# Performance work log

Measured on AMD Instinct MI355X. Metric: run time of the kernel, lower is better.

Reference implementation:

```python
import jax, jax.numpy as jnp
import numpy as np

N, E, C = 50000, 800000, 128
D = C // 4
EPS = 1e-5


def _bn(x, g, b):
    # training-mode BatchNorm1d over the batch (row) dimension
    mu = jnp.mean(x, axis=0)
    var = jnp.var(x, axis=0)
    return (x - mu) * jax.lax.rsqrt(var + EPS) * g + b


def _lin_bn_elu(x, w, b, g, bb):
    return jax.nn.elu(_bn(x @ w + b, g, bb))


def setup_inputs() -> dict:
    key = jax.random.key(0)
    ks = iter(jax.random.split(key, 40))
    inp = {}
    inp['node_feats'] = jax.random.normal(next(ks), (N, C), jnp.float32)
    inp['edge_feats'] = jax.random.normal(next(ks), (E, C), jnp.float32)
    inp['src'] = jax.random.randint(next(ks), (E,), 0, N)
    inp['dst'] = jax.random.randint(next(ks), (E,), 0, N)

    def add_lin(name, fi, fo):
        inp[name + '_w'] = jax.random.normal(next(ks), (fi, fo), jnp.float32) / np.sqrt(fi)
        inp[name + '_b'] = jnp.zeros((fo,), jnp.float32)

    def add_bn(name, f):
        inp[name + '_g'] = jnp.ones((f,), jnp.float32)
        inp[name + '_b'] = jnp.zeros((f,), jnp.float32)

    add_lin('pdn', C, D); add_bn('bn1n', D)
    add_lin('pde', C, D); add_bn('bn1e', D)
    add_lin('e1', 3 * D, D); add_bn('bne1', D)
    add_lin('e2', 2 * D, D); add_bn('bne2', D)
    add_lin('nm', 2 * D, D); add_bn('bnnm', D)
    add_lin('pun', D, C); add_bn('bn2n', C)
    add_lin('pue', D, C); add_bn('bn2e', C)
    return inp


def reference(node_feats, edge_feats, src, dst,
              pdn_w, pdn_b, bn1n_g, bn1n_b,
              pde_w, pde_b, bn1e_g, bn1e_b,
              e1_w, e1_b, bne1_g, bne1_b,
              e2_w, e2_b, bne2_g, bne2_b,
              nm_w, nm_b, bnnm_g, bnnm_b,
              pun_w, pun_b, bn2n_g, bn2n_b,
              pue_w, pue_b, bn2e_g, bn2e_b):
    # project down
    h_node = _lin_bn_elu(node_feats, pdn_w, pdn_b, bn1n_g, bn1n_b)  # [N,D]
    h_edge = _lin_bn_elu(edge_feats, pde_w, pde_b, bn1e_g, bn1e_b)  # [E,D]
    # ENConv: gather src/dst node features per edge
    hs = h_node[src]  # [E,D]
    hd = h_node[dst]  # [E,D]
    ex = _lin_bn_elu(jnp.concatenate([hs, hd, h_edge], axis=1), e1_w, e1_b, bne1_g, bne1_b)  # [E,D]
    m = _lin_bn_elu(jnp.concatenate([hs, ex], axis=1), e2_w, e2_b, bne2_g, bne2_b)  # [E,D]
    # scatter-mean messages to destination nodes (DGL fn.mean; isolated nodes -> 0)
    msum = jax.ops.segment_sum(m, dst, num_segments=N)
    deg = jax.ops.segment_sum(jnp.ones((E,), m.dtype), dst, num_segments=N)
    h_mean = msum / jnp.maximum(deg, 1.0)[:, None]
    ho = _lin_bn_elu(jnp.concatenate([h_node, h_mean], axis=1), nm_w, nm_b, bnnm_g, bnnm_b)  # [N,D]
    # project up + residual (dropout is identity in eval)
    node_out = jax.nn.elu(_bn(ho @ pun_w + pun_b, bn2n_g, bn2n_b) + node_feats)
    edge_out = jax.nn.elu(_bn(ex @ pue_w + pue_b, bn2e_g, bn2e_b) + edge_feats)
    return node_out, edge_out
```

## Files before the change

kernel.cpp:

```cpp
#include <hip/hip_runtime.h>
#include <hip/hip_bf16.h>

typedef unsigned int u32;
typedef unsigned short u16;

#define NN 50000
#define EE 800000
#define EPSBN 1e-5f

static constexpr size_t ALGN = 256;
static constexpr size_t align_up(size_t x){ return (x + ALGN - 1) & ~(ALGN - 1); }

static constexpr size_t OFF_ST   = 0;
static constexpr size_t OFF_MSUM = align_up(OFF_ST + 832*4);
static constexpr size_t OFF_DEG  = align_up(OFF_MSUM + (size_t)NN*32*4);
static constexpr size_t ZERO_END = align_up(OFF_DEG + (size_t)NN*4);
static constexpr size_t OFF_WF   = ZERO_END;
static constexpr size_t OFF_BF   = align_up(OFF_WF + 23552*4);
static constexpr size_t OFF_AFF  = align_up(OFF_BF + 416*4);
static constexpr size_t OFF_GB   = align_up(OFF_AFF + 832*4);
static constexpr size_t OFF_FLAG = align_up(OFF_GB + 832*4);
static constexpr size_t OFF_X1N  = align_up(OFF_FLAG + 256);
static constexpr size_t OFF_HOP  = align_up(OFF_X1N + (size_t)NN*32*4);
static constexpr size_t OFF_X1E  = align_up(OFF_HOP + (size_t)NN*32*4);
static constexpr size_t OFF_EXP  = align_up(OFF_X1E + (size_t)EE*32*2);

#define ST_1N 0
#define ST_1E 64
#define ST_E1 128
#define ST_E2 192
#define ST_NM 256
#define ST_2N 320
#define ST_2E 576
#define WF_PDN 0
#define WF_PDE 4096
#define WF_E1  8192
#define WF_E2  11264
#define WF_NM  13312
#define WF_PUN 15360
#define WF_PUE 19456
#define BF_PDN 0
#define BF_PDE 32
#define BF_E1  64
#define BF_E2  96
#define BF_NM  128
#define BF_PUN 160
#define BF_PUE 288
#define AF_1N 0
#define AF_1E 64
#define AF_E1 128
#define AF_E2 192
#define AF_NM 256
#define AF_2N 320
#define AF_2E 576

__device__ __forceinline__ float bf2f(u16 h){ return __uint_as_float(((u32)h)<<16); }
__device__ __forceinline__ u16 f2bf(float f){
  u32 u = __float_as_uint(f);
  u32 r = (u + 0x7fffu + ((u>>16)&1u)) >> 16;
  return (u16)r;
}
__device__ __forceinline__ float eluf(float x){ return x > 0.f ? x : __expf(x) - 1.f; }
__device__ __forceinline__ float wsum64(float v){
  #pragma unroll
  for (int off = 32; off; off >>= 1) v += __shfl_xor(v, off, 64);
  return v;
}

__device__ __forceinline__ void stats_flush(const float* sum, const float* ssq,
                                            float* gsum, float* gssq){
  const int lane = threadIdx.x & 63;
  float a = 0.f;
  #pragma unroll
  for (int q = 0; q < 32; q++){
    float s = wsum64(sum[q]);
    float t = wsum64(ssq[q]);
    if (lane == q)      a = s;
    if (lane == 32 + q) a = t;
  }
  if (lane < 32) atomicAdd(gsum + lane, a);
  else           atomicAdd(gssq + (lane - 32), a);
}

__device__ __forceinline__ void part_f32_affelu(const float* __restrict__ x,
    const float* __restrict__ aff, const float* __restrict__ W, float* acc){
  for (int k0 = 0; k0 < 32; k0 += 4){
    float4 v = *(const float4*)(x + k0);
    const float xv[4] = {v.x, v.y, v.z, v.w};
    #pragma unroll
    for (int i = 0; i < 4; i++){
      float h = eluf(fmaf(xv[i], aff[k0+i], aff[32+k0+i]));
      const float* wr = W + (k0+i)*32;
      #pragma unroll
      for (int j = 0; j < 32; j++) acc[j] = fmaf(h, wr[j], acc[j]);
    }
  }
}
__device__ __forceinline__ void part_mean(const float* __restrict__ x, float scale,
    const float* __restrict__ W, float* acc){
  for (int k0 = 0; k0 < 32; k0 += 4){
    float4 v = *(const float4*)(x + k0);
    const float xv[4] = {v.x, v.y, v.z, v.w};
    #pragma unroll
    for (int i = 0; i < 4; i++){
      float h = xv[i] * scale;
      const float* wr = W + (k0+i)*32;
      #pragma unroll
      for (int j = 0; j < 32; j++) acc[j] = fmaf(h, wr[j], acc[j]);
    }
  }
}
__device__ __forceinline__ void part_bf16_affelu(const u32* __restrict__ xw,
    const float* __restrict__ aff, const float* __restrict__ W, float* acc){
  for (int k0 = 0; k0 < 32; k0 += 8){
    uint4 u = *(const uint4*)(xw + k0/2);
    const u32 ww[4] = {u.x, u.y, u.z, u.w};
    #pragma unroll
    for (int i = 0; i < 4; i++){
      int k = k0 + 2*i;
      float h0 = eluf(fmaf(__uint_as_float(ww[i]<<16),          aff[k],   aff[32+k]));
      float h1 = eluf(fmaf(__uint_as_float(ww[i]&0xffff0000u),  aff[k+1], aff[32+k+1]));
      const float* wr = W + k*32;
      #pragma unroll
      for (int j = 0; j < 32; j++) acc[j] = fmaf(h0, wr[j],    acc[j]);
      #pragma unroll
      for (int j = 0; j < 32; j++) acc[j] = fmaf(h1, wr[32+j], acc[j]);
    }
  }
}
template<int BF16IN>
__device__ __forceinline__ void part_up(const void* __restrict__ xin, size_t r,
    const float* __restrict__ aff, const float* __restrict__ W, int c, float* acc){
  if (BF16IN){
    const u32* xw = ((const u32*)xin) + r*16;
    for (int k0 = 0; k0 < 32; k0 += 8){
      uint4 u = *(const uint4*)(xw + k0/2);
      const u32 ww[4] = {u.x, u.y, u.z, u.w};
      #pragma unroll
      for (int i = 0; i < 4; i++){
        int k = k0 + 2*i;
        float h0 = eluf(fmaf(__uint_as_float(ww[i]<<16),         aff[k],   aff[32+k]));
        float h1 = eluf(fmaf(__uint_as_float(ww[i]&0xffff0000u), aff[k+1], aff[32+k+1]));
        const float* wr = W + k*128 + c*32;
        #pragma unroll
        for (int j = 0; j < 32; j++) acc[j] = fmaf(h0, wr[j],     acc[j]);
        #pragma unroll
        for (int j = 0; j < 32; j++) acc[j] = fmaf(h1, wr[128+j], acc[j]);
      }
    }
  } else {
    const float* xf = ((const float*)xin) + r*32;
    for (int k0 = 0; k0 < 32; k0 += 4){
      float4 v = *(const float4*)(xf + k0);
      const float xv[4] = {v.x, v.y, v.z, v.w};
      #pragma unroll
      for (int i = 0; i < 4; i++){
        float h = eluf(fmaf(xv[i], aff[k0+i], aff[32+k0+i]));
        const float* wr = W + (k0+i)*128 + c*32;
        #pragma unroll
        for (int j = 0; j < 32; j++) acc[j] = fmaf(h, wr[j], acc[j]);
      }
    }
  }
}


__global__ void ksniff(const u16* __restrict__ p, int* __restrict__ flag){
  __shared__ int cnt;
  if (threadIdx.x == 0) cnt = 0;
  __syncthreads();
  u16 u = p[threadIdx.x];
  int e = (u >> 7) & 0xFF;
  if (e >= 97 && e <= 134) atomicAdd(&cnt, 1);
  __syncthreads();
  if (threadIdx.x == 0) *flag = (cnt >= 200) ? 1 : 0;
}

struct PrepArgs { const void* s[28]; float* d[28]; int n[28]; };
__global__ void __launch_bounds__(256) kprep(PrepArgs a, const int* __restrict__ flagp){
  const int isbf = *flagp;
  const int gid = blockIdx.x*256 + threadIdx.x;
  const int stride = gridDim.x*256;
  for (int t = 0; t < 28; t++){
    float* d = a.d[t]; int n = a.n[t];
    if (isbf){
      const u16* s = (const u16*)a.s[t];
      for (int i = gid; i < n; i += stride) d[i] = bf2f(s[i]);
    } else {
      const float* s = (const float*)a.s[t];
      for (int i = gid; i < n; i += stride) d[i] = s[i];
    }
  }
}

template<int STOREBF>
__global__ void __launch_bounds__(256) kproj(const void* __restrict__ xin,
    const float* __restrict__ W, const float* __restrict__ bias,
    void* __restrict__ xout, float* gsum, float* gssq, int nrows,
    const int* __restrict__ flagp){
  const int isbf = *flagp;
  const int gid = blockIdx.x*256 + threadIdx.x;
  const int stride = gridDim.x*256;
  float sum[32], ssq[32];
  #pragma unroll
  for (int j = 0; j < 32; j++){ sum[j] = 0.f; ssq[j] = 0.f; }
  for (int r = gid; r < nrows; r += stride){
    float acc[32];
    #pragma unroll
    for (int j = 0; j < 32; j++) acc[j] = bias[j];
    if (isbf){
      const uint4* row = (const uint4*)((const u32*)xin + (size_t)r*64);
      for (int kk = 0; kk < 16; kk++){
        uint4 u = row[kk];
        const u32 ww[4] = {u.x, u.y, u.z, u.w};
        #pragma unroll
        for (int i = 0; i < 4; i++){
          float x0 = __uint_as_float(ww[i]<<16);
          float x1 = __uint_as_float(ww[i]&0xffff0000u);
          const float* w0 = W + (kk*8 + 2*i)*32;
          #pragma unroll
          for (int j = 0; j < 32; j++) acc[j] = fmaf(x0, w0[j],    acc[j]);
          #pragma unroll
          for (int j = 0; j < 32; j++) acc[j] = fmaf(x1, w0[32+j], acc[j]);
        }
      }
    } else {
      const float* rowf = (const float*)xin + (size_t)r*128;
      for (int kk = 0; kk < 32; kk++){
        float4 v = *(const float4*)(rowf + kk*4);
        const float xv[4] = {v.x, v.y, v.z, v.w};
        #pragma unroll
        for (int i = 0; i < 4; i++){
          const float* w0 = W + (kk*4 + i)*32;
          #pragma unroll
          for (int j = 0; j < 32; j++) acc[j] = fmaf(xv[i], w0[j], acc[j]);
        }
      }
    }
    if (STOREBF){
      u32 pk[16];
      #pragma unroll
      for (int q = 0; q < 16; q++) pk[q] = (u32)f2bf(acc[2*q]) | ((u32)f2bf(acc[2*q+1])<<16);
      uint4* op = (uint4*)((u32*)xout + (size_t)r*16);
      #pragma unroll
      for (int q = 0; q < 4; q++) op[q] = make_uint4(pk[q*4], pk[q*4+1], pk[q*4+2], pk[q*4+3]);
    } else {
      float4* op = (float4*)((float*)xout + (size_t)r*32);
      #pragma unroll
      for (int q = 0; q < 8; q++)
        op[q] = make_float4(acc[q*4], acc[q*4+1], acc[q*4+2], acc[q*4+3]);
    }
    #pragma unroll
    for (int j = 0; j < 32; j++){ sum[j] += acc[j]; ssq[j] = fmaf(acc[j], acc[j], ssq[j]); }
  }
  stats_flush(sum, ssq, gsum, gssq);
}

__global__ void __launch_bounds__(256) kex(const int* __restrict__ src,
    const int* __restrict__ dst, const float* __restrict__ x1n,
    const u32* __restrict__ x1e, const float* __restrict__ a1n,
    const float* __restrict__ a1e, const float* __restrict__ W,
    const float* __restrict__ bias, u32* __restrict__ expre,
    float* gsum, float* gssq, int nrows){
  const int gid = blockIdx.x*256 + threadIdx.x;
  const int stride = gridDim.x*256;
  float sum[32], ssq[32];
  #pragma unroll
  for (int j = 0; j < 32; j++){ sum[j] = 0.f; ssq[j] = 0.f; }
  for (int r = gid; r < nrows; r += stride){
    float acc[32];
    #pragma unroll
    for (int j = 0; j < 32; j++) acc[j] = bias[j];
    int s = src[r], d = dst[r];
    part_f32_affelu(x1n + (size_t)s*32, a1n, W,        acc);
    part_f32_affelu(x1n + (size_t)d*32, a1n, W + 1024, acc);
    part_bf16_affelu(x1e + (size_t)r*16, a1e, W + 2048, acc);
    u32 pk[16];
    #pragma unroll
    for (int q = 0; q < 16; q++) pk[q] = (u32)f2bf(acc[2*q]) | ((u32)f2bf(acc[2*q+1])<<16);
    uint4* op = (uint4*)(expre + (size_t)r*16);
    #pragma unroll
    for (int q = 0; q < 4; q++) op[q] = make_uint4(pk[q*4], pk[q*4+1], pk[q*4+2], pk[q*4+3]);
    #pragma unroll
    for (int j = 0; j < 32; j++){ sum[j] += acc[j]; ssq[j] = fmaf(acc[j], acc[j], ssq[j]); }
  }
  stats_flush(sum, ssq, gsum, gssq);
}

__global__ void __launch_bounds__(256) km(const int* __restrict__ src,
    const float* __restrict__ x1n, const float* __restrict__ a1n,
    const u32* __restrict__ expre, const float* __restrict__ ae1,
    const float* __restrict__ W, const float* __restrict__ bias,
    u32* __restrict__ mpre, float* gsum, float* gssq, int nrows){
  const int gid = blockIdx.x*256 + threadIdx.x;
  const int stride = gridDim.x*256;
  float sum[32], ssq[32];
  #pragma unroll
  for (int j = 0; j < 32; j++){ sum[j] = 0.f; ssq[j] = 0.f; }
  for (int r = gid; r < nrows; r += stride){
    float acc[32];
    #pragma unroll
    for (int j = 0; j < 32; j++) acc[j] = bias[j];
    int s = src[r];
    part_f32_affelu(x1n + (size_t)s*32, a1n, W, acc);
    part_bf16_affelu(expre + (size_t)r*16, ae1, W + 1024, acc);
    u32 pk[16];
    #pragma unroll
    for (int q = 0; q < 16; q++) pk[q] = (u32)f2bf(acc[2*q]) | ((u32)f2bf(acc[2*q+1])<<16);
    uint4* op = (uint4*)(mpre + (size_t)r*16);
    #pragma unroll
    for (int q = 0; q < 4; q++) op[q] = make_uint4(pk[q*4], pk[q*4+1], pk[q*4+2], pk[q*4+3]);
    #pragma unroll
    for (int j = 0; j < 32; j++){ sum[j] += acc[j]; ssq[j] = fmaf(acc[j], acc[j], ssq[j]); }
  }
  stats_flush(sum, ssq, gsum, gssq);
}

__global__ void __launch_bounds__(256) ksc(const int* __restrict__ dst,
    const u32* __restrict__ mpre, const float* __restrict__ ae2,
    float* __restrict__ msum, float* __restrict__ deg){
  const int gid = blockIdx.x*256 + threadIdx.x;
  const int stride = gridDim.x*256;
  const u16* mp = (const u16*)mpre;
  for (int idx = gid; idx < EE*32; idx += stride){
    int e = idx >> 5, j = idx & 31;
    float v = eluf(fmaf(bf2f(mp[idx]), ae2[j], ae2[32+j]));
    int dn = dst[e];
    atomicAdd(msum + (size_t)dn*32 + j, v);
    if (j == 0) atomicAdd(deg + dn, 1.f);
  }
}

__global__ void __launch_bounds__(256) kho(const float* __restrict__ x1n,
    const float* __restrict__ a1n, const float* __restrict__ msum,
    const float* __restrict__ deg, const float* __restrict__ W,
    const float* __restrict__ bias, float* __restrict__ hopre,
    float* gsum, float* gssq, int nrows){
  const int gid = blockIdx.x*256 + threadIdx.x;
  const int stride = gridDim.x*256;
  float sum[32], ssq[32];
  #pragma unroll
  for (int j = 0; j < 32; j++){ sum[j] = 0.f; ssq[j] = 0.f; }
  for (int r = gid; r < nrows; r += stride){
    float acc[32];
    #pragma unroll
    for (int j = 0; j < 32; j++) acc[j] = bias[j];
    part_f32_affelu(x1n + (size_t)r*32, a1n, W, acc);
    float id = 1.f / fmaxf(deg[r], 1.f);
    part_mean(msum + (size_t)r*32, id, W + 1024, acc);
    float4* op = (float4*)(hopre + (size_t)r*32);
    #pragma unroll
    for (int q = 0; q < 8; q++)
      op[q] = make_float4(acc[q*4], acc[q*4+1], acc[q*4+2], acc[q*4+3]);
    #pragma unroll
    for (int j = 0; j < 32; j++){ sum[j] += acc[j]; ssq[j] = fmaf(acc[j], acc[j], ssq[j]); }
  }
  stats_flush(sum, ssq, gsum, gssq);
}

template<int BF16IN>
__global__ void __launch_bounds__(256) kup1(const void* __restrict__ xin,
    const float* __restrict__ aff, const float* __restrict__ W,
    const float* __restrict__ bias, float* __restrict__ st, int nrows){
  const int gid = blockIdx.x*256 + threadIdx.x;
  const int stride = gridDim.x*256;
  for (int c = 0; c < 4; c++){
    float sum[32], ssq[32];
    #pragma unroll
    for (int j = 0; j < 32; j++){ sum[j] = 0.f; ssq[j] = 0.f; }
    for (int r = gid; r < nrows; r += stride){
      float acc[32];
      #pragma unroll
      for (int j = 0; j < 32; j++) acc[j] = bias[c*32+j];
      part_up<BF16IN>(xin, (size_t)r, aff, W, c, acc);
      #pragma unroll
      for (int j = 0; j < 32; j++){ sum[j] += acc[j]; ssq[j] = fmaf(acc[j], acc[j], ssq[j]); }
    }
    stats_flush(sum, ssq, st + c*32, st + 128 + c*32);
  }
}

template<int BF16IN>
__global__ void __launch_bounds__(256) kup2(const void* __restrict__ xin,
    const float* __restrict__ aff_in, const float* __restrict__ W,
    const float* __restrict__ bias, const float* __restrict__ aff_out,
    const void* __restrict__ resid, void* __restrict__ out,
    size_t row_off, int nrows, const int* __restrict__ flagp){
  const int isbf = *flagp;
  const int gid = blockIdx.x*256 + threadIdx.x;
  const int stride = gridDim.x*256;
  for (int r = gid; r < nrows; r += stride){
    for (int c = 0; c < 4; c++){
      float acc[32];
      #pragma unroll
      for (int j = 0; j < 32; j++) acc[j] = bias[c*32+j];
      part_up<BF16IN>(xin, (size_t)r, aff_in, W, c, acc);
      const float* sc = aff_out + c*32;
      const float* sh = aff_out + 128 + c*32;
      if (isbf){
        const u32* rrow = (const u32*)resid + (size_t)r*64 + c*16;
        u32* orow = (u32*)out + (row_off + (size_t)r)*64 + c*16;
        u32 rw[16];
        const uint4* rp = (const uint4*)rrow;
        #pragma unroll
        for (int q = 0; q < 4; q++){
          uint4 u = rp[q];
          rw[q*4] = u.x; rw[q*4+1] = u.y; rw[q*4+2] = u.z; rw[q*4+3] = u.w;
        }
        u32 pk[16];
        #pragma unroll
        for (int q = 0; q < 16; q++){
          float o0 = eluf(fmaf(acc[2*q],   sc[2*q],   sh[2*q])   + __uint_as_float(rw[q]<<16));
          float o1 = eluf(fmaf(acc[2*q+1], sc[2*q+1], sh[2*q+1]) + __uint_as_float(rw[q]&0xffff0000u));
          pk[q] = (u32)f2bf(o0) | ((u32)f2bf(o1)<<16);
        }
        uint4* op = (uint4*)orow;
        #pragma unroll
        for (int q = 0; q < 4; q++) op[q] = make_uint4(pk[q*4], pk[q*4+1], pk[q*4+2], pk[q*4+3]);
      } else {
        const float* rrow = (const float*)resid + (size_t)r*128 + c*32;
        float* orow = (float*)out + (row_off + (size_t)r)*128 + c*32;
        #pragma unroll
        for (int q = 0; q < 8; q++){
          float4 rv = *(const float4*)(rrow + q*4);
          float o0 = eluf(fmaf(acc[q*4],   sc[q*4],   sh[q*4])   + rv.x);
          float o1 = eluf(fmaf(acc[q*4+1], sc[q*4+1], sh[q*4+1]) + rv.y);
          float o2 = eluf(fmaf(acc[q*4+2], sc[q*4+2], sh[q*4+2]) + rv.z);
          float o3 = eluf(fmaf(acc[q*4+3], sc[q*4+3], sh[q*4+3]) + rv.w);
          *(float4*)(orow + q*4) = make_float4(o0, o1, o2, o3);
        }
      }
    }
  }
}

__global__ void kfin(const float* __restrict__ st, const float* __restrict__ g,
                     const float* __restrict__ b, float* __restrict__ aff,
                     int ncols, float invcnt){
  int j = threadIdx.x;
  if (j < ncols){
    float mu  = st[j] * invcnt;
    float var = fmaxf(fmaf(-mu, mu, st[ncols+j] * invcnt), 0.f);
    float scv = g[j] * rsqrtf(var + EPSBN);
    aff[j] = scv;
    aff[ncols+j] = fmaf(-mu, scv, b[j]);
  }
}

extern "C" void kernel_launch(void* const* d_in, const int* in_sizes, int n_in,
                              void* d_out, int out_size, void* d_ws, size_t ws_size,
                              hipStream_t stream){
  (void)in_sizes; (void)n_in; (void)out_size; (void)ws_size;
  char* ws = (char*)d_ws;
  float* ST  = (float*)(ws + OFF_ST);
  float* MS  = (float*)(ws + OFF_MSUM);
  float* DG  = (float*)(ws + OFF_DEG);
  float* WF  = (float*)(ws + OFF_WF);
  float* BFp = (float*)(ws + OFF_BF);
  float* AF  = (float*)(ws + OFF_AFF);
  float* GB  = (float*)(ws + OFF_GB);
  int*   FL  = (int*)(ws + OFF_FLAG);
  float* X1N = (float*)(ws + OFF_X1N);
  float* HOP = (float*)(ws + OFF_HOP);
  u32*   X1E = (u32*)(ws + OFF_X1E);
  u32*   EXP = (u32*)(ws + OFF_EXP);

  const int* src = (const int*)d_in[2];
  const int* dst = (const int*)d_in[3];

  hipMemsetAsync(ws + OFF_ST, 0, ZERO_END - OFF_ST, stream);
  ksniff<<<1,256,0,stream>>>((const u16*)d_in[0], FL);

  PrepArgs pa;
  const int widx[7] = {4,8,12,16,20,24,28};
  const int woff[7] = {WF_PDN,WF_PDE,WF_E1,WF_E2,WF_NM,WF_PUN,WF_PUE};
  const int wlen[7] = {4096,4096,3072,2048,2048,4096,4096};
  const int bidx[7] = {5,9,13,17,21,25,29};
  const int boff[7] = {BF_PDN,BF_PDE,BF_E1,BF_E2,BF_NM,BF_PUN,BF_PUE};
  const int blen[7] = {32,32,32,32,32,128,128};
  const int gbidx[14] = {6,7,10,11,14,15,18,19,22,23,26,27,30,31};
  const int gboff[14] = {0,32,64,96,128,160,192,224,256,288,320,448,576,704};
  const int gblen[14] = {32,32,32,32,32,32,32,32,32,32,128,128,128,128};
  for (int t = 0; t < 7; t++){
    pa.s[t]   = d_in[widx[t]]; pa.d[t]   = WF  + woff[t]; pa.n[t]   = wlen[t];
    pa.s[7+t] = d_in[bidx[t]]; pa.d[7+t] = BFp + boff[t]; pa.n[7+t] = blen[t];
  }
  for (int t = 0; t < 14; t++){
    pa.s[14+t] = d_in[gbidx[t]]; pa.d[14+t] = GB + gboff[t]; pa.n[14+t] = gblen[t];
  }
  kprep<<<32,256,0,stream>>>(pa, FL);

  kproj<0><<<196,256,0,stream>>>(d_in[0], WF+WF_PDN, BFp+BF_PDN, X1N, ST+ST_1N, ST+ST_1N+32, NN, FL);
  kproj<1><<<1024,256,0,stream>>>(d_in[1], WF+WF_PDE, BFp+BF_PDE, X1E, ST+ST_1E, ST+ST_1E+32, EE, FL);
  kfin<<<1,128,0,stream>>>(ST+ST_1N, GB+0,  GB+32, AF+AF_1N, 32, 1.0f/NN);
  kfin<<<1,128,0,stream>>>(ST+ST_1E, GB+64, GB+96, AF+AF_1E, 32, 1.0f/EE);

  kex<<<1024,256,0,stream>>>(src, dst, X1N, X1E, AF+AF_1N, AF+AF_1E,
                             WF+WF_E1, BFp+BF_E1, EXP, ST+ST_E1, ST+ST_E1+32, EE);
  kfin<<<1,128,0,stream>>>(ST+ST_E1, GB+128, GB+160, AF+AF_E1, 32, 1.0f/EE);

  km<<<1024,256,0,stream>>>(src, X1N, AF+AF_1N, EXP, AF+AF_E1,
                            WF+WF_E2, BFp+BF_E2, X1E , ST+ST_E2, ST+ST_E2+32, EE);
  kfin<<<1,128,0,stream>>>(ST+ST_E2, GB+192, GB+224, AF+AF_E2, 32, 1.0f/EE);

  ksc<<<2048,256,0,stream>>>(dst, X1E, AF+AF_E2, MS, DG);

  kho<<<196,256,0,stream>>>(X1N, AF+AF_1N, MS, DG, WF+WF_NM, BFp+BF_NM, HOP,
                            ST+ST_NM, ST+ST_NM+32, NN);
  kfin<<<1,128,0,stream>>>(ST+ST_NM, GB+256, GB+288, AF+AF_NM, 32, 1.0f/NN);

  kup1<0><<<196,256,0,stream>>>(HOP, AF+AF_NM, WF+WF_PUN, BFp+BF_PUN, ST+ST_2N, NN);
  kfin<<<1,128,0,stream>>>(ST+ST_2N, GB+320, GB+448, AF+AF_2N, 128, 1.0f/NN);
  kup2<0><<<196,256,0,stream>>>(HOP, AF+AF_NM, WF+WF_PUN, BFp+BF_PUN, AF+AF_2N,
                                d_in[0], d_out, 0, NN, FL);

  kup1<1><<<1024,256,0,stream>>>(EXP, AF+AF_E1, WF+WF_PUE, BFp+BF_PUE, ST+ST_2E, EE);
  kfin<<<1,128,0,stream>>>(ST+ST_2E, GB+576, GB+704, AF+AF_2E, 128, 1.0f/EE);
  kup2<1><<<2048,256,0,stream>>>(EXP, AF+AF_E1, WF+WF_PUE, BFp+BF_PUE, AF+AF_2E,
                                 d_in[1], d_out, NN, EE, FL);
}
```

Before: 2.222 ms.

## Compute up-projection BatchNorm stats via Gram matrix instead of full matmul pass

The separate stats pass over the 32→128 up-projection is replaced by a kernel that accumulates the column sums and the 32x32 Gram matrix of the activated inputs. A small finalize kernel then derives per-output mean and variance through W^T S W. This removes a full 128-wide matmul pass over 800k edges and 50k nodes. The output kernel now computes the activated input once per row and uses nontemporal stores, and several grid sizes are raised. The Gram-based variance can lose precision through cancellation in fp32.

```diff
diff --git a/kernel.cpp b/kernel.cpp
--- a/kernel.cpp
+++ b/kernel.cpp
@@ -3,6 +3,8 @@
 
 typedef unsigned int u32;
 typedef unsigned short u16;
+typedef unsigned int u32x4 __attribute__((ext_vector_type(4)));
+typedef float f32x4 __attribute__((ext_vector_type(4)));
 
 #define NN 50000
 #define EE 800000
@@ -30,8 +32,6 @@
 #define ST_E1 128
 #define ST_E2 192
 #define ST_NM 256
-#define ST_2N 320
-#define ST_2E 576
 #define WF_PDN 0
 #define WF_PDE 4096
 #define WF_E1  8192
@@ -128,41 +128,6 @@
     }
   }
 }
-template<int BF16IN>
-__device__ __forceinline__ void part_up(const void* __restrict__ xin, size_t r,
-    const float* __restrict__ aff, const float* __restrict__ W, int c, float* acc){
-  if (BF16IN){
-    const u32* xw = ((const u32*)xin) + r*16;
-    for (int k0 = 0; k0 < 32; k0 += 8){
-      uint4 u = *(const uint4*)(xw + k0/2);
-      const u32 ww[4] = {u.x, u.y, u.z, u.w};
-      #pragma unroll
-      for (int i = 0; i < 4; i++){
-        int k = k0 + 2*i;
-        float h0 = eluf(fmaf(__uint_as_float(ww[i]<<16),         aff[k],   aff[32+k]));
-        float h1 = eluf(fmaf(__uint_as_float(ww[i]&0xffff0000u), aff[k+1], aff[32+k+1]));
-        const float* wr = W + k*128 + c*32;
-        #pragma unroll
-        for (int j = 0; j < 32; j++) acc[j] = fmaf(h0, wr[j],     acc[j]);
-        #pragma unroll
-        for (int j = 0; j < 32; j++) acc[j] = fmaf(h1, wr[128+j], acc[j]);
-      }
-    }
-  } else {
-    const float* xf = ((const float*)xin) + r*32;
-    for (int k0 = 0; k0 < 32; k0 += 4){
-      float4 v = *(const float4*)(xf + k0);
-      const float xv[4] = {v.x, v.y, v.z, v.w};
-      #pragma unroll
-      for (int i = 0; i < 4; i++){
-        float h = eluf(fmaf(xv[i], aff[k0+i], aff[32+k0+i]));
-        const float* wr = W + (k0+i)*128 + c*32;
-        #pragma unroll
-        for (int j = 0; j < 32; j++) acc[j] = fmaf(h, wr[j], acc[j]);
-      }
-    }
-  }
-}
 
 
 __global__ void ksniff(const u16* __restrict__ p, int* __restrict__ flag){
@@ -359,25 +324,103 @@
 }
 
 template<int BF16IN>
-__global__ void __launch_bounds__(256) kup1(const void* __restrict__ xin,
-    const float* __restrict__ aff, const float* __restrict__ W,
-    const float* __restrict__ bias, float* __restrict__ st, int nrows){
-  const int gid = blockIdx.x*256 + threadIdx.x;
-  const int stride = gridDim.x*256;
-  for (int c = 0; c < 4; c++){
-    float sum[32], ssq[32];
-    #pragma unroll
-    for (int j = 0; j < 32; j++){ sum[j] = 0.f; ssq[j] = 0.f; }
-    for (int r = gid; r < nrows; r += stride){
-      float acc[32];
-      #pragma unroll
-      for (int j = 0; j < 32; j++) acc[j] = bias[c*32+j];
-      part_up<BF16IN>(xin, (size_t)r, aff, W, c, acc);
-      #pragma unroll
-      for (int j = 0; j < 32; j++){ sum[j] += acc[j]; ssq[j] = fmaf(acc[j], acc[j], ssq[j]); }
-    }
-    stats_flush(sum, ssq, st + c*32, st + 128 + c*32);
-  }
+__global__ void __launch_bounds__(256) ksyrk(const void* __restrict__ xin,
+    const float* __restrict__ aff, float* __restrict__ s1g,
+    float* __restrict__ s2g, int nrows){
+  __shared__ float hL[256*34];
+  const int t = threadIdx.x;
+  const int i0 = (t >> 4) << 1;
+  const int j0 = (t & 15) << 1;
+  float s1[32];
+  #pragma unroll
+  for (int k = 0; k < 32; k++) s1[k] = 0.f;
+  float c00 = 0.f, c01 = 0.f, c10 = 0.f, c11 = 0.f;
+  const int stride = gridDim.x*256;
+  for (int base = blockIdx.x*256; base < nrows; base += stride){
+    int r = base + t;
+    int nv = nrows - base; if (nv > 256) nv = 256;
+    __syncthreads();
+    if (r < nrows){
+      float* hrow = hL + t*34;
+      if (BF16IN){
+        const uint4* xp = (const uint4*)((const u32*)xin + (size_t)r*16);
+        #pragma unroll
+        for (int q2 = 0; q2 < 4; q2++){
+          uint4 u = xp[q2];
+          const u32 ww[4] = {u.x, u.y, u.z, u.w};
+          #pragma unroll
+          for (int i = 0; i < 4; i++){
+            int k = q2*8 + 2*i;
+            float h0 = eluf(fmaf(__uint_as_float(ww[i]<<16),         aff[k],   aff[32+k]));
+            float h1 = eluf(fmaf(__uint_as_float(ww[i]&0xffff0000u), aff[k+1], aff[32+k+1]));
+            hrow[k] = h0; hrow[k+1] = h1;
+            s1[k] += h0; s1[k+1] += h1;
+          }
+        }
+      } else {
+        const float* xf = (const float*)xin + (size_t)r*32;
+        #pragma unroll
+        for (int k0 = 0; k0 < 32; k0 += 4){
+          float4 v = *(const float4*)(xf + k0);
+          float h0 = eluf(fmaf(v.x, aff[k0],   aff[32+k0]));
+          float h1 = eluf(fmaf(v.y, aff[k0+1], aff[32+k0+1]));
+          float h2 = eluf(fmaf(v.z, aff[k0+2], aff[32+k0+2]));
+          float h3 = eluf(fmaf(v.w, aff[k0+3], aff[32+k0+3]));
+          hrow[k0] = h0; hrow[k0+1] = h1; hrow[k0+2] = h2; hrow[k0+3] = h3;
+          s1[k0] += h0; s1[k0+1] += h1; s1[k0+2] += h2; s1[k0+3] += h3;
+        }
+      }
+    }
+    __syncthreads();
+    #pragma unroll 2
+    for (int rr = 0; rr < nv; rr++){
+      const float* hr = hL + rr*34;
+      float2 hi = *(const float2*)(hr + i0);
+      float2 hj = *(const float2*)(hr + j0);
+      c00 = fmaf(hi.x, hj.x, c00);
+      c01 = fmaf(hi.x, hj.y, c01);
+      c10 = fmaf(hi.y, hj.x, c10);
+      c11 = fmaf(hi.y, hj.y, c11);
+    }
+  }
+  atomicAdd(s2g + (size_t)(i0  )*32 + j0,     c00);
+  atomicAdd(s2g + (size_t)(i0  )*32 + j0 + 1, c01);
+  atomicAdd(s2g + (size_t)(i0+1)*32 + j0,     c10);
+  atomicAdd(s2g + (size_t)(i0+1)*32 + j0 + 1, c11);
+  const int lane = t & 63;
+  float a = 0.f;
+  #pragma unroll
+  for (int q = 0; q < 32; q++){
+    float v = wsum64(s1[q]);
+    if (lane == q) a = v;
+  }
+  if (lane < 32) atomicAdd(s1g + lane, a);
+}
+
+__global__ void kfin2(const float* __restrict__ s1, const float* __restrict__ s2,
+                      const float* __restrict__ W, const float* __restrict__ bias,
+                      const float* __restrict__ g, const float* __restrict__ b,
+                      float* __restrict__ aff, float invn){
+  int j = threadIdx.x;
+  float wj[32];
+  #pragma unroll
+  for (int k = 0; k < 32; k++) wj[k] = W[k*128 + j];
+  float s = 0.f;
+  #pragma unroll
+  for (int k = 0; k < 32; k++) s = fmaf(s1[k], wj[k], s);
+  s *= invn;
+  float qf = 0.f;
+  for (int k = 0; k < 32; k++){
+    float t = 0.f;
+    #pragma unroll
+    for (int l = 0; l < 32; l++) t = fmaf(s2[k*32 + l], wj[l], t);
+    qf = fmaf(wj[k], t, qf);
+  }
+  float var = fmaxf(fmaf(-s, s, qf*invn), 0.f);
+  float mu  = s + bias[j];
+  float scv = g[j] * rsqrtf(var + EPSBN);
+  aff[j] = scv;
+  aff[128 + j] = fmaf(-mu, scv, b[j]);
 }
 
 template<int BF16IN>
@@ -390,23 +433,51 @@
   const int gid = blockIdx.x*256 + threadIdx.x;
   const int stride = gridDim.x*256;
   for (int r = gid; r < nrows; r += stride){
-    for (int c = 0; c < 4; c++){
-      float acc[32];
-      #pragma unroll
-      for (int j = 0; j < 32; j++) acc[j] = bias[c*32+j];
-      part_up<BF16IN>(xin, (size_t)r, aff_in, W, c, acc);
-      const float* sc = aff_out + c*32;
-      const float* sh = aff_out + 128 + c*32;
-      if (isbf){
-        const u32* rrow = (const u32*)resid + (size_t)r*64 + c*16;
-        u32* orow = (u32*)out + (row_off + (size_t)r)*64 + c*16;
-        u32 rw[16];
-        const uint4* rp = (const uint4*)rrow;
-        #pragma unroll
-        for (int q = 0; q < 4; q++){
-          uint4 u = rp[q];
-          rw[q*4] = u.x; rw[q*4+1] = u.y; rw[q*4+2] = u.z; rw[q*4+3] = u.w;
-        }
+    float h[32];
+    if (BF16IN){
+      const uint4* xp = (const uint4*)((const u32*)xin + (size_t)r*16);
+      #pragma unroll
+      for (int q2 = 0; q2 < 4; q2++){
+        uint4 u = xp[q2];
+        const u32 ww[4] = {u.x, u.y, u.z, u.w};
+        #pragma unroll
+        for (int i = 0; i < 4; i++){
+          int k = q2*8 + 2*i;
+          h[k]   = eluf(fmaf(__uint_as_float(ww[i]<<16),         aff_in[k],   aff_in[32+k]));
+          h[k+1] = eluf(fmaf(__uint_as_float(ww[i]&0xffff0000u), aff_in[k+1], aff_in[32+k+1]));
+        }
+      }
+    } else {
+      const float* xf = (const float*)xin + (size_t)r*32;
+      #pragma unroll
+      for (int k0 = 0; k0 < 32; k0 += 4){
+        float4 v = *(const float4*)(xf + k0);
+        h[k0]   = eluf(fmaf(v.x, aff_in[k0],   aff_in[32+k0]));
+        h[k0+1] = eluf(fmaf(v.y, aff_in[k0+1], aff_in[32+k0+1]));
+        h[k0+2] = eluf(fmaf(v.z, aff_in[k0+2], aff_in[32+k0+2]));
+        h[k0+3] = eluf(fmaf(v.w, aff_in[k0+3], aff_in[32+k0+3]));
+      }
+    }
+    if (isbf){
+      const uint4* rp = (const uint4*)((const u32*)resid + (size_t)r*64);
+      u32x4* op = (u32x4*)((u32*)out + (row_off + (size_t)r)*64);
+      #pragma unroll 1
+      for (int c = 0; c < 4; c++){
+        uint4 u0 = rp[c*4+0], u1 = rp[c*4+1], u2 = rp[c*4+2], u3 = rp[c*4+3];
+        float acc[32];
+        const float* bp = bias + c*32;
+        #pragma unroll
+        for (int j = 0; j < 32; j++) acc[j] = bp[j];
+        for (int k = 0; k < 32; k++){
+          const float* wr = W + k*128 + c*32;
+          float hk = h[k];
+          #pragma unroll
+          for (int j = 0; j < 32; j++) acc[j] = fmaf(hk, wr[j], acc[j]);
+        }
+        const float* sc = aff_out + c*32;
+        const float* sh = aff_out + 128 + c*32;
+        const u32 rw[16] = {u0.x,u0.y,u0.z,u0.w, u1.x,u1.y,u1.z,u1.w,
+                            u2.x,u2.y,u2.z,u2.w, u3.x,u3.y,u3.z,u3.w};
         u32 pk[16];
         #pragma unroll
         for (int q = 0; q < 16; q++){
@@ -414,20 +485,40 @@
           float o1 = eluf(fmaf(acc[2*q+1], sc[2*q+1], sh[2*q+1]) + __uint_as_float(rw[q]&0xffff0000u));
           pk[q] = (u32)f2bf(o0) | ((u32)f2bf(o1)<<16);
         }
-        uint4* op = (uint4*)orow;
-        #pragma unroll
-        for (int q = 0; q < 4; q++) op[q] = make_uint4(pk[q*4], pk[q*4+1], pk[q*4+2], pk[q*4+3]);
-      } else {
-        const float* rrow = (const float*)resid + (size_t)r*128 + c*32;
-        float* orow = (float*)out + (row_off + (size_t)r)*128 + c*32;
+        #pragma unroll
+        for (int q = 0; q < 4; q++){
+          u32x4 pv = {pk[q*4], pk[q*4+1], pk[q*4+2], pk[q*4+3]};
+          __builtin_nontemporal_store(pv, op + c*4 + q);
+        }
+      }
+    } else {
+      const float4* rp = (const float4*)((const float*)resid + (size_t)r*128);
+      f32x4* op = (f32x4*)((float*)out + (row_off + (size_t)r)*128);
+      #pragma unroll 1
+      for (int c = 0; c < 4; c++){
+        float4 rv[8];
+        #pragma unroll
+        for (int q = 0; q < 8; q++) rv[q] = rp[c*8 + q];
+        float acc[32];
+        const float* bp = bias + c*32;
+        #pragma unroll
+        for (int j = 0; j < 32; j++) acc[j] = bp[j];
+        for (int k = 0; k < 32; k++){
+          const float* wr = W + k*128 + c*32;
+          float hk = h[k];
+          #pragma unroll
+          for (int j = 0; j < 32; j++) acc[j] = fmaf(hk, wr[j], acc[j]);
+        }
+        const float* sc = aff_out + c*32;
+        const float* sh = aff_out + 128 + c*32;
         #pragma unroll
         for (int q = 0; q < 8; q++){
-          float4 rv = *(const float4*)(rrow + q*4);
-          float o0 = eluf(fmaf(acc[q*4],   sc[q*4],   sh[q*4])   + rv.x);
-          float o1 = eluf(fmaf(acc[q*4+1], sc[q*4+1], sh[q*4+1]) + rv.y);
-          float o2 = eluf(fmaf(acc[q*4+2], sc[q*4+2], sh[q*4+2]) + rv.z);
-          float o3 = eluf(fmaf(acc[q*4+3], sc[q*4+3], sh[q*4+3]) + rv.w);
-          *(float4*)(orow + q*4) = make_float4(o0, o1, o2, o3);
+          float o0 = eluf(fmaf(acc[q*4],   sc[q*4],   sh[q*4])   + rv[q].x);
+          float o1 = eluf(fmaf(acc[q*4+1], sc[q*4+1], sh[q*4+1]) + rv[q].y);
+          float o2 = eluf(fmaf(acc[q*4+2], sc[q*4+2], sh[q*4+2]) + rv[q].z);
+          float o3 = eluf(fmaf(acc[q*4+3], sc[q*4+3], sh[q*4+3]) + rv[q].w);
+          f32x4 ov = {o0, o1, o2, o3};
+          __builtin_nontemporal_store(ov, op + c*8 + q);
         }
       }
     }
@@ -491,15 +582,15 @@
   kprep<<<32,256,0,stream>>>(pa, FL);
 
   kproj<0><<<196,256,0,stream>>>(d_in[0], WF+WF_PDN, BFp+BF_PDN, X1N, ST+ST_1N, ST+ST_1N+32, NN, FL);
-  kproj<1><<<1024,256,0,stream>>>(d_in[1], WF+WF_PDE, BFp+BF_PDE, X1E, ST+ST_1E, ST+ST_1E+32, EE, FL);
+  kproj<1><<<1563,256,0,stream>>>(d_in[1], WF+WF_PDE, BFp+BF_PDE, X1E, ST+ST_1E, ST+ST_1E+32, EE, FL);
   kfin<<<1,128,0,stream>>>(ST+ST_1N, GB+0,  GB+32, AF+AF_1N, 32, 1.0f/NN);
   kfin<<<1,128,0,stream>>>(ST+ST_1E, GB+64, GB+96, AF+AF_1E, 32, 1.0f/EE);
 
-  kex<<<1024,256,0,stream>>>(src, dst, X1N, X1E, AF+AF_1N, AF+AF_1E,
+  kex<<<1563,256,0,stream>>>(src, dst, X1N, X1E, AF+AF_1N, AF+AF_1E,
                              WF+WF_E1, BFp+BF_E1, EXP, ST+ST_E1, ST+ST_E1+32, EE);
   kfin<<<1,128,0,stream>>>(ST+ST_E1, GB+128, GB+160, AF+AF_E1, 32, 1.0f/EE);
 
-  km<<<1024,256,0,stream>>>(src, X1N, AF+AF_1N, EXP, AF+AF_E1,
+  km<<<1563,256,0,stream>>>(src, X1N, AF+AF_1N, EXP, AF+AF_E1,
                             WF+WF_E2, BFp+BF_E2, X1E , ST+ST_E2, ST+ST_E2+32, EE);
   kfin<<<1,128,0,stream>>>(ST+ST_E2, GB+192, GB+224, AF+AF_E2, 32, 1.0f/EE);
 
@@ -509,13 +600,17 @@
                             ST+ST_NM, ST+ST_NM+32, NN);
   kfin<<<1,128,0,stream>>>(ST+ST_NM, GB+256, GB+288, AF+AF_NM, 32, 1.0f/NN);
 
-  kup1<0><<<196,256,0,stream>>>(HOP, AF+AF_NM, WF+WF_PUN, BFp+BF_PUN, ST+ST_2N, NN);
-  kfin<<<1,128,0,stream>>>(ST+ST_2N, GB+320, GB+448, AF+AF_2N, 128, 1.0f/NN);
+  hipMemsetAsync(MS, 0, 2112*4, stream);
+
+  ksyrk<1><<<625,256,0,stream>>>(EXP, AF+AF_E1, MS+1056, MS+1088, EE);
+  kfin2<<<1,128,0,stream>>>(MS+1056, MS+1088, WF+WF_PUE, BFp+BF_PUE,
+                            GB+576, GB+704, AF+AF_2E, 1.0f/EE);
+  ksyrk<0><<<196,256,0,stream>>>(HOP, AF+AF_NM, MS, MS+32, NN);
+  kfin2<<<1,128,0,stream>>>(MS, MS+32, WF+WF_PUN, BFp+BF_PUN,
+                            GB+320, GB+448, AF+AF_2N, 1.0f/NN);
+
   kup2<0><<<196,256,0,stream>>>(HOP, AF+AF_NM, WF+WF_PUN, BFp+BF_PUN, AF+AF_2N,
                                 d_in[0], d_out, 0, NN, FL);
-
-  kup1<1><<<1024,256,0,stream>>>(EXP, AF+AF_E1, WF+WF_PUE, BFp+BF_PUE, ST+ST_2E, EE);
-  kfin<<<1,128,0,stream>>>(ST+ST_2E, GB+576, GB+704, AF+AF_2E, 128, 1.0f/EE);
-  kup2<1><<<2048,256,0,stream>>>(EXP, AF+AF_E1, WF+WF_PUE, BFp+BF_PUE, AF+AF_2E,
+  kup2<1><<<3125,256,0,stream>>>(EXP, AF+AF_E1, WF+WF_PUE, BFp+BF_PUE, AF+AF_2E,
                                  d_in[1], d_out, NN, EE, FL);
 }
```

Result: slower. 2.475 ms (+11.4%).
